# Performance work log

Measured on AMD Instinct MI355X. Metric: run time of the kernel, lower is better.

Reference implementation:

```python
import jax, jax.numpy as jnp
import numpy as np

N_NODES = 50000
N_GRAPHS = 64


def gcn_conv(x, W, b, row, col, norm, n):
    # PyG GCNConv: h = x @ W; out[i] = sum_{(j,i) in E+selfloops} norm_ji * h[j] + b
    h = x @ W
    msg = norm[:, None] * h[row]
    out = jax.ops.segment_sum(msg, col, num_segments=n)
    return out + b


def setup_inputs() -> dict:
    key = jax.random.key(0)
    ks = jax.random.split(key, 12)
    F_in, H, C = 128, 128, 16
    x = jax.random.normal(ks[0], (N_NODES, F_in), dtype=jnp.float32)
    edge_index = jax.random.randint(ks[1], (2, 800000), 0, N_NODES, dtype=jnp.int64)
    batch = jnp.sort(jax.random.randint(ks[2], (N_NODES,), 0, N_GRAPHS, dtype=jnp.int64))
    def glorot(k, shape):
        lim = np.sqrt(6.0 / (shape[0] + shape[1]))
        return jax.random.uniform(k, shape, jnp.float32, -lim, lim)
    return {
        "x": x,
        "edge_index": edge_index,
        "batch": batch,
        "W0": glorot(ks[3], (F_in, H)), "b0": jnp.zeros((H,), jnp.float32),
        "W1": glorot(ks[4], (H, H)),   "b1": jnp.zeros((H,), jnp.float32),
        "W2": glorot(ks[5], (H, H)),   "b2": jnp.zeros((H,), jnp.float32),
        "lin_W": glorot(ks[6], (H, C)),
        "lin_b": jnp.zeros((C,), jnp.float32),
    }


def reference(x, edge_index, batch, W0, b0, W1, b1, W2, b2, lin_W, lin_b):
    n = x.shape[0]
    # add self-loops
    loops = jnp.arange(n, dtype=edge_index.dtype)
    row = jnp.concatenate([edge_index[0], loops])
    col = jnp.concatenate([edge_index[1], loops])
    # symmetric normalization: deg over destination (col) incl. self-loops
    deg = jax.ops.segment_sum(jnp.ones_like(col, dtype=x.dtype), col, num_segments=n)
    dinv = jnp.where(deg > 0, jax.lax.rsqrt(deg), 0.0)
    norm = dinv[row] * dinv[col]

    h = gcn_conv(x, W0, b0, row, col, norm, n)
    h = jax.nn.relu(h)
    h = gcn_conv(h, W1, b1, row, col, norm, n)
    h = jax.nn.relu(h)
    h = gcn_conv(h, W2, b2, row, col, norm, n)

    # global mean pool over graphs
    sums = jax.ops.segment_sum(h, batch, num_segments=N_GRAPHS)
    cnts = jax.ops.segment_sum(jnp.ones((n,), h.dtype), batch, num_segments=N_GRAPHS)
    pooled = sums / jnp.maximum(cnts, 1.0)[:, None]

    # dropout is identity in eval mode
    logits = pooled @ lin_W + lin_b
    return jax.nn.softmax(logits, axis=1)
```

## Files before the change

### kernel.cpp

```cpp
#include <hip/hip_runtime.h>


#define NF 128
#define MAXBUCK 512
#define CAP 2560
#define L1_CHUNK 4096
#define L1_THREADS 512
#define L1_PER_THREAD 8
#define PPG 8

typedef __attribute__((ext_vector_type(8))) short short8;
typedef __attribute__((ext_vector_type(4))) float floatx4;
typedef __attribute__((ext_vector_type(2))) float floatx2;

__device__ __forceinline__ unsigned int bf16_rne(float x) {
    unsigned int u = __float_as_uint(x);
    return (u + 0x7fffu + ((u >> 16) & 1u)) >> 16;
}
__device__ __forceinline__ unsigned int pack_bf16_rne(float x, float y) {
    return bf16_rne(x) | (bf16_rne(y) << 16);
}
__device__ __forceinline__ float bf16u_to_f32(unsigned int u) {
    return __uint_as_float(u << 16);
}

__global__ __launch_bounds__(256) void k_repack_w3(const float* __restrict__ W0,
                                                   const float* __restrict__ W1,
                                                   const float* __restrict__ W2,
                                                   unsigned short* __restrict__ whi,
                                                   unsigned short* __restrict__ wlo,
                                                   int* __restrict__ bucket_cursor) {
    if (blockIdx.x == 0) {
        for (int i = threadIdx.x; i <= MAXBUCK; i += 256) bucket_cursor[i] = 0;
    }
    int wsel = blockIdx.x >> 3;
    const float* W = (wsel == 0) ? W0 : (wsel == 1) ? W1 : W2;
    int idx = (blockIdx.x & 7) * 256 + threadIdx.x;
    int slab = wsel * NF * NF;
    int l = idx & 63;
    int t = (idx >> 6) & 7;
    int s = idx >> 9;
    int kbase = s * 32 + (l >> 4) * 8;
    int nn = t * 16 + (l & 15);
    #pragma unroll
    for (int j = 0; j < 8; ++j) {
        float w = W[(kbase + j) * NF + nn];
        unsigned int h = bf16_rne(w);
        float hf = __uint_as_float(h << 16);
        unsigned int lo = bf16_rne(w - hf);
        whi[slab + idx * 8 + j] = (unsigned short)h;
        wlo[slab + idx * 8 + j] = (unsigned short)lo;
    }
}

__global__ __launch_bounds__(L1_THREADS) void k_bucket_scatter(
        const int* __restrict__ row, const int* __restrict__ colv,
        int* __restrict__ bucket_cursor, unsigned int* __restrict__ buck_arr,
        int ne, int etot, int nbuck) {
    __shared__ unsigned int hist[MAXBUCK];
    __shared__ unsigned int lbase[MAXBUCK];
    __shared__ unsigned int lcur[MAXBUCK];
    __shared__ unsigned int runb[MAXBUCK];
    __shared__ unsigned int sa[MAXBUCK], sb[MAXBUCK];
    __shared__ unsigned int reorder[L1_CHUNK];
    int t = threadIdx.x;
    int e0 = blockIdx.x * L1_CHUNK;
    int cnt_here = min(etot - e0, L1_CHUNK);

    hist[t] = 0;
    __syncthreads();

    unsigned int myv[L1_PER_THREAD];
    #pragma unroll
    for (int j = 0; j < L1_PER_THREAD; ++j) {
        int e = e0 + j * L1_THREADS + t;
        if (e < etot) {
            int s, d;
            if (e < ne) { s = row[e]; d = colv[e]; } else { s = d = e - ne; }
            myv[j] = (unsigned int)s | ((unsigned int)d << 16);
            atomicAdd(&hist[d >> 7], 1u);
        } else myv[j] = 0xffffffffu;
    }
    __syncthreads();

    sa[t] = hist[t];
    __syncthreads();
    unsigned int* pin = sa;
    unsigned int* pout = sb;
    #pragma unroll
    for (int off = 1; off < MAXBUCK; off <<= 1) {
        pout[t] = pin[t] + ((t >= off) ? pin[t - off] : 0);
        __syncthreads();
        unsigned int* tmp = pin; pin = pout; pout = tmp;
    }
    unsigned int ex = pin[t] - hist[t];
    lbase[t] = ex;
    lcur[t]  = ex;
    if (t < nbuck && hist[t] > 0)
        runb[t] = (unsigned int)atomicAdd(&bucket_cursor[t], (int)hist[t]);
    __syncthreads();

    #pragma unroll
    for (int j = 0; j < L1_PER_THREAD; ++j) {
        unsigned int v = myv[j];
        if (v != 0xffffffffu) {
            unsigned int p = atomicAdd(&lcur[v >> 23], 1u);
            reorder[p] = v;
        }
    }
    __syncthreads();

    for (int i = t; i < cnt_here; i += L1_THREADS) {
        unsigned int v = reorder[i];
        unsigned int b = v >> 23;
        buck_arr[(size_t)b * CAP + runb[b] + ((unsigned int)i - lbase[b])] = v;
    }
}

__global__ __launch_bounds__(256) void k_fine(const unsigned int* __restrict__ buck_arr,
                                              const int* __restrict__ bucket_cursor,
                                              int* __restrict__ starts,
                                              int* __restrict__ ends,
                                              float* __restrict__ dinv,
                                              unsigned short* __restrict__ src16,
                                              int n) {
    int b = blockIdx.x;
    int base = b * CAP;
    int m = min(bucket_cursor[b], CAP);
    int node0 = b << 7;
    int nn = min(128, n - node0);
    __shared__ unsigned int cnt[128];
    __shared__ unsigned int lsc[256];
    __shared__ unsigned int lcur[128];
    __shared__ unsigned short srcbuf[CAP];
    int t = threadIdx.x;
    if (t < 128) cnt[t] = 0;
    __syncthreads();
    for (int i = t; i < m; i += 256)
        atomicAdd(&cnt[(buck_arr[base + i] >> 16) - node0], 1u);
    __syncthreads();
    unsigned int v0 = (t < 128) ? cnt[t] : 0;
    lsc[t] = v0;
    __syncthreads();
    #pragma unroll
    for (int off = 1; off < 128; off <<= 1) {
        unsigned int add = (t >= off) ? lsc[t - off] : 0;
        __syncthreads();
        lsc[t] += add;
        __syncthreads();
    }
    if (t < 128) {
        unsigned int ex = lsc[t] - v0;
        lcur[t] = ex;
        if (t < nn) {
            starts[node0 + t] = base + (int)ex;
            ends[node0 + t]   = base + (int)(ex + v0);
            dinv[node0 + t]   = rsqrtf((float)v0);
        }
    }
    __syncthreads();
    for (int i = t; i < m; i += 256) {
        unsigned int v = buck_arr[base + i];
        unsigned int p = atomicAdd(&lcur[(v >> 16) - node0], 1u);
        srcbuf[p] = (unsigned short)(v & 0xffffu);
    }
    __syncthreads();
    for (int i = t; i < m; i += 256)
        src16[base + i] = srcbuf[i];
}

__global__ __launch_bounds__(256) void k_gemm_mfma(const float* __restrict__ Af,
                                                   const unsigned short* __restrict__ Ab,
                                                   const unsigned short* __restrict__ Whi,
                                                   const unsigned short* __restrict__ Wlo,
                                                   const float* __restrict__ dinv,
                                                   unsigned char* __restrict__ Out,
                                                   int M) {
    __shared__ unsigned short As[128 * 136];
    int tid = threadIdx.x;
    int row0 = blockIdx.x * 128;

    if (Af) {
        for (int c = tid; c < 2048; c += 256) {
            int r = c >> 4, off = c & 15;
            int gr = min(row0 + r, M - 1);
            const float4* p = (const float4*)(Af + (size_t)gr * NF) + off * 2;
            float4 v0 = p[0], v1 = p[1];
            uint4 pk;
            pk.x = pack_bf16_rne(v0.x, v0.y);
            pk.y = pack_bf16_rne(v0.z, v0.w);
            pk.z = pack_bf16_rne(v1.x, v1.y);
            pk.w = pack_bf16_rne(v1.z, v1.w);
            *(uint4*)(&As[r * 136 + off * 8]) = pk;
        }
    } else {
        for (int c = tid; c < 2048; c += 256) {
            int r = c >> 4, off = c & 15;
            int gr = min(row0 + r, M - 1);
            *(uint4*)(&As[r * 136 + off * 8]) = ((const uint4*)(Ab + (size_t)gr * NF))[off];
        }
    }
    __syncthreads();

    int wave = tid >> 6, l = tid & 63;
    int q = l >> 4, c16 = l & 15;
    int wrow0 = wave * 16;

    floatx4 acc[2][8];
    #pragma unroll
    for (int h = 0; h < 2; ++h)
        #pragma unroll
        for (int t = 0; t < 8; ++t) acc[h][t] = (floatx4){0.f, 0.f, 0.f, 0.f};

    #pragma unroll
    for (int s = 0; s < 4; ++s) {
        short8 a0 = *(const short8*)(&As[(wrow0 + c16) * 136 + s * 32 + q * 8]);
        short8 a1 = *(const short8*)(&As[(64 + wrow0 + c16) * 136 + s * 32 + q * 8]);
        #pragma unroll
        for (int t = 0; t < 8; ++t) {
            short8 bh = *(const short8*)(Whi + ((size_t)((s * 8 + t) * 64 + l) * 8));
            short8 bl = *(const short8*)(Wlo + ((size_t)((s * 8 + t) * 64 + l) * 8));
            acc[0][t] = __builtin_amdgcn_mfma_f32_16x16x32_bf16(a0, bh, acc[0][t], 0, 0, 0);
            acc[0][t] = __builtin_amdgcn_mfma_f32_16x16x32_bf16(a0, bl, acc[0][t], 0, 0, 0);
            acc[1][t] = __builtin_amdgcn_mfma_f32_16x16x32_bf16(a1, bh, acc[1][t], 0, 0, 0);
            acc[1][t] = __builtin_amdgcn_mfma_f32_16x16x32_bf16(a1, bl, acc[1][t], 0, 0, 0);
        }
    }

    #pragma unroll
    for (int h = 0; h < 2; ++h) {
        float ds[4];
        #pragma unroll
        for (int i = 0; i < 4; ++i) {
            int gr = row0 + h * 64 + wrow0 + q * 4 + i;
            ds[i] = (gr < M) ? dinv[gr] : 0.f;
        }
        #pragma unroll
        for (int t = 0; t < 8; ++t) {
            #pragma unroll
            for (int i = 0; i < 4; ++i) {
                int gr = row0 + h * 64 + wrow0 + q * 4 + i;
                if (gr < M) {
                    float v = acc[h][t][i] * ds[i];
                    unsigned int pk = __builtin_amdgcn_cvt_pk_fp8_f32(v, v, 0, false);
                    Out[(size_t)gr * NF + t * 16 + c16] = (unsigned char)(pk & 0xffu);
                }
            }
        }
    }
}

__global__ __launch_bounds__(256) void k_agg_fp8(const unsigned char* __restrict__ hs8,
                                                 const int* __restrict__ starts,
                                                 const int* __restrict__ ends,
                                                 const unsigned short* __restrict__ src16,
                                                 const float* __restrict__ dinv,
                                                 const float* __restrict__ bias,
                                                 unsigned short* __restrict__ out,
                                                 int n, int do_relu) {
    int wave = threadIdx.x >> 6;
    int lane = threadIdx.x & 63;
    int node = blockIdx.x * 4 + wave;
    if (node >= n) return;
    int g = lane >> 4;
    int f = lane & 15;
    int start = starts[node], end = ends[node];

    const uint2* h2 = (const uint2*)hs8;
    float acc[8];
    #pragma unroll
    for (int j = 0; j < 8; ++j) acc[j] = 0.f;

    for (int base = start; base < end; base += 32) {
        int   sidx[8];
        float msk[8];
        #pragma unroll
        for (int j = 0; j < 8; ++j) {
            int e = base + g + 4 * j;
            bool v = e < end;
            sidx[j] = (int)src16[v ? e : start];
            msk[j]  = v ? 1.f : 0.f;
        }
        uint2 rr[8];
        #pragma unroll
        for (int j = 0; j < 8; ++j)
            rr[j] = h2[(size_t)sidx[j] * 16 + f];
        #pragma unroll
        for (int j = 0; j < 8; ++j) {
            float m = msk[j];
            floatx2 p0 = __builtin_amdgcn_cvt_pk_f32_fp8(rr[j].x, false);
            floatx2 p1 = __builtin_amdgcn_cvt_pk_f32_fp8(rr[j].x, true);
            floatx2 p2 = __builtin_amdgcn_cvt_pk_f32_fp8(rr[j].y, false);
            floatx2 p3 = __builtin_amdgcn_cvt_pk_f32_fp8(rr[j].y, true);
            acc[0] = fmaf(m, p0.x, acc[0]);
            acc[1] = fmaf(m, p0.y, acc[1]);
            acc[2] = fmaf(m, p1.x, acc[2]);
            acc[3] = fmaf(m, p1.y, acc[3]);
            acc[4] = fmaf(m, p2.x, acc[4]);
            acc[5] = fmaf(m, p2.y, acc[5]);
            acc[6] = fmaf(m, p3.x, acc[6]);
            acc[7] = fmaf(m, p3.y, acc[7]);
        }
    }

    #pragma unroll
    for (int j = 0; j < 8; ++j) {
        acc[j] += __shfl_xor(acc[j], 16);
        acc[j] += __shfl_xor(acc[j], 32);
    }

    if (g == 0) {
        float dd = dinv[node];
        float4 b0 = ((const float4*)bias)[2 * f];
        float4 b1 = ((const float4*)bias)[2 * f + 1];
        float r[8];
        r[0] = fmaf(dd, acc[0], b0.x); r[1] = fmaf(dd, acc[1], b0.y);
        r[2] = fmaf(dd, acc[2], b0.z); r[3] = fmaf(dd, acc[3], b0.w);
        r[4] = fmaf(dd, acc[4], b1.x); r[5] = fmaf(dd, acc[5], b1.y);
        r[6] = fmaf(dd, acc[6], b1.z); r[7] = fmaf(dd, acc[7], b1.w);
        if (do_relu) {
            #pragma unroll
            for (int j = 0; j < 8; ++j) r[j] = fmaxf(r[j], 0.f);
        }
        uint4 pk;
        pk.x = pack_bf16_rne(r[0], r[1]);
        pk.y = pack_bf16_rne(r[2], r[3]);
        pk.z = pack_bf16_rne(r[4], r[5]);
        pk.w = pack_bf16_rne(r[6], r[7]);
        ((uint4*)out)[(size_t)node * 16 + f] = pk;
    }
}

__global__ __launch_bounds__(128) void k_pool_partial(const unsigned short* __restrict__ h,
                                                      const int* __restrict__ batch,
                                                      float* __restrict__ pooled_part,
                                                      int n) {
    __shared__ float red[8][NF];
    int b = blockIdx.x;
    int g = b / PPG;
    int j = b % PPG;
    int t = threadIdx.x;

    int lo = 0, hi = n;
    while (lo < hi) { int mid = (lo + hi) >> 1; if (batch[mid] < g) lo = mid + 1; else hi = mid; }
    int s = lo;
    lo = s; hi = n;
    while (lo < hi) { int mid = (lo + hi) >> 1; if (batch[mid] < g + 1) lo = mid + 1; else hi = mid; }
    int e = lo;

    int len = e - s;
    int chunk = (len + PPG - 1) / PPG;
    int i0 = s + j * chunk;
    int i1 = min(e, i0 + chunk);

    int r = t >> 4, f8 = t & 15;
    float acc[8];
    #pragma unroll
    for (int k = 0; k < 8; ++k) acc[k] = 0.f;
    for (int i = i0 + r; i < i1; i += 8) {
        uint4 v = *(const uint4*)(&h[(size_t)i * NF + f8 * 8]);
        acc[0] += bf16u_to_f32(v.x & 0xffffu); acc[1] += bf16u_to_f32(v.x >> 16);
        acc[2] += bf16u_to_f32(v.y & 0xffffu); acc[3] += bf16u_to_f32(v.y >> 16);
        acc[4] += bf16u_to_f32(v.z & 0xffffu); acc[5] += bf16u_to_f32(v.z >> 16);
        acc[6] += bf16u_to_f32(v.w & 0xffffu); acc[7] += bf16u_to_f32(v.w >> 16);
    }
    #pragma unroll
    for (int k = 0; k < 8; ++k) red[r][f8 * 8 + k] = acc[k];
    __syncthreads();
    float ssum = 0.f;
    #pragma unroll
    for (int rr = 0; rr < 8; ++rr) ssum += red[rr][t];
    pooled_part[(size_t)b * NF + t] = ssum;
}

__global__ __launch_bounds__(1024) void k_head(const float* __restrict__ pooled_part,
                                               const int* __restrict__ batch,
                                               const float* __restrict__ linW,
                                               const float* __restrict__ linb,
                                               float* __restrict__ out,
                                               int n, int n_graphs) {
    __shared__ float ph[64 * NF];
    int t = threadIdx.x;
    for (int i = t; i < n_graphs * NF; i += 1024) {
        int g = i >> 7, f = i & 127;
        float s = 0.f;
        #pragma unroll
        for (int j = 0; j < PPG; ++j)
            s += pooled_part[(size_t)(g * PPG + j) * NF + f];
        ph[i] = s;
    }
    __syncthreads();

    int g = t >> 4;
    int c = t & 15;

    int lo = 0, hi = n;
    while (lo < hi) { int mid = (lo + hi) >> 1; if (batch[mid] < g) lo = mid + 1; else hi = mid; }
    int start = lo;
    lo = start; hi = n;
    while (lo < hi) { int mid = (lo + hi) >> 1; if (batch[mid] < g + 1) lo = mid + 1; else hi = mid; }
    float inv_cnt = 1.f / fmaxf((float)(lo - start), 1.f);

    float acc = linb[c];
    for (int k = 0; k < NF; ++k)
        acc += ph[g * NF + k] * inv_cnt * linW[k * 16 + c];

    float m = acc;
    #pragma unroll
    for (int s2 = 8; s2 >= 1; s2 >>= 1) m = fmaxf(m, __shfl_xor(m, s2, 16));
    float e = expf(acc - m);
    float ssum = e;
    #pragma unroll
    for (int s2 = 8; s2 >= 1; s2 >>= 1) ssum += __shfl_xor(ssum, s2, 16);
    out[g * 16 + c] = e / ssum;
}

extern "C" void kernel_launch(void* const* d_in, const int* in_sizes, int n_in,
                              void* d_out, int out_size, void* d_ws, size_t ws_size,
                              hipStream_t stream) {
    const float* x    = (const float*)d_in[0];
    const int*   edge = (const int*)d_in[1];
    const int*   batch= (const int*)d_in[2];
    const float* W0   = (const float*)d_in[3];
    const float* b0   = (const float*)d_in[4];
    const float* W1   = (const float*)d_in[5];
    const float* b1   = (const float*)d_in[6];
    const float* W2   = (const float*)d_in[7];
    const float* b2   = (const float*)d_in[8];
    const float* linW = (const float*)d_in[9];
    const float* linb = (const float*)d_in[10];

    int n  = in_sizes[0] / NF;
    int ne = in_sizes[1] / 2;
    int n_graphs = out_size / 16;
    const int* row  = edge;
    const int* colv = edge + ne;
    int etot = ne + n;
    int nbuck = (n + 127) >> 7;

    char* p = (char*)d_ws;
    auto alloc = [&](size_t bytes) { char* r = p; p += (bytes + 255) & ~(size_t)255; return r; };
    int*   bucket_cursor = (int*)alloc((size_t)(MAXBUCK + 1) * 4);
    unsigned int* buck_arr = (unsigned int*)alloc((size_t)MAXBUCK * CAP * 4);
    unsigned short* src16  = (unsigned short*)alloc((size_t)MAXBUCK * CAP * 2);
    int*   starts  = (int*)  alloc((size_t)n * 4);
    int*   ends    = (int*)  alloc((size_t)n * 4);
    float* dinv    = (float*)alloc((size_t)n * 4);
    unsigned char*  gbuf8 = (unsigned char*) alloc((size_t)n * NF);
    unsigned short* abuf  = (unsigned short*)alloc((size_t)n * NF * 2);
    float* pooled_part = (float*)alloc((size_t)n_graphs * PPG * NF * 4);
    unsigned short* whi = (unsigned short*)alloc((size_t)3 * NF * NF * 2);
    unsigned short* wlo = (unsigned short*)alloc((size_t)3 * NF * NF * 2);

    k_repack_w3<<<24, 256, 0, stream>>>(W0, W1, W2, whi, wlo, bucket_cursor);

    k_bucket_scatter<<<(etot + L1_CHUNK - 1) / L1_CHUNK, L1_THREADS, 0, stream>>>(
        row, colv, bucket_cursor, buck_arr, ne, etot, nbuck);
    k_fine<<<nbuck, 256, 0, stream>>>(buck_arr, bucket_cursor, starts, ends, dinv, src16, n);

    int gemm_blocks = (n + 127) / 128;
    int agg_blocks  = (n + 3) / 4;
    const size_t WSLAB = (size_t)NF * NF;

    k_gemm_mfma<<<gemm_blocks, 256, 0, stream>>>(x, nullptr, whi, wlo, dinv, gbuf8, n);
    k_agg_fp8  <<<agg_blocks, 256, 0, stream>>>(gbuf8, starts, ends, src16, dinv, b0, abuf, n, 1);
    k_gemm_mfma<<<gemm_blocks, 256, 0, stream>>>(nullptr, abuf, whi + WSLAB, wlo + WSLAB, dinv, gbuf8, n);
    k_agg_fp8  <<<agg_blocks, 256, 0, stream>>>(gbuf8, starts, ends, src16, dinv, b1, abuf, n, 1);
    k_gemm_mfma<<<gemm_blocks, 256, 0, stream>>>(nullptr, abuf, whi + 2 * WSLAB, wlo + 2 * WSLAB, dinv, gbuf8, n);
    k_agg_fp8  <<<agg_blocks, 256, 0, stream>>>(gbuf8, starts, ends, src16, dinv, b2, abuf, n, 0);

    k_pool_partial<<<n_graphs * PPG, 128, 0, stream>>>(abuf, batch, pooled_part, n);
    k_head<<<1, 1024, 0, stream>>>(pooled_part, batch, linW, linb, (float*)d_out, n, n_graphs);
}
```

Baseline: 277.2 us.

## Fuse CSR finalize with first GEMM and merge pooling with head

```diff
diff --git a/kernel.cpp b/kernel.cpp
--- a/kernel.cpp
+++ b/kernel.cpp
@@ -7,7 +7,6 @@
 #define L1_CHUNK 4096
 #define L1_THREADS 512
 #define L1_PER_THREAD 8
-#define PPG 8
 
 typedef __attribute__((ext_vector_type(8))) short short8;
 typedef __attribute__((ext_vector_type(4))) float floatx4;
@@ -117,68 +116,15 @@
     }
 }
 
-__global__ __launch_bounds__(256) void k_fine(const unsigned int* __restrict__ buck_arr,
-                                              const int* __restrict__ bucket_cursor,
-                                              int* __restrict__ starts,
-                                              int* __restrict__ ends,
-                                              float* __restrict__ dinv,
-                                              unsigned short* __restrict__ src16,
-                                              int n) {
-    int b = blockIdx.x;
-    int base = b * CAP;
-    int m = min(bucket_cursor[b], CAP);
-    int node0 = b << 7;
-    int nn = min(128, n - node0);
-    __shared__ unsigned int cnt[128];
-    __shared__ unsigned int lsc[256];
-    __shared__ unsigned int lcur[128];
-    __shared__ unsigned short srcbuf[CAP];
-    int t = threadIdx.x;
-    if (t < 128) cnt[t] = 0;
-    __syncthreads();
-    for (int i = t; i < m; i += 256)
-        atomicAdd(&cnt[(buck_arr[base + i] >> 16) - node0], 1u);
-    __syncthreads();
-    unsigned int v0 = (t < 128) ? cnt[t] : 0;
-    lsc[t] = v0;
-    __syncthreads();
-    #pragma unroll
-    for (int off = 1; off < 128; off <<= 1) {
-        unsigned int add = (t >= off) ? lsc[t - off] : 0;
-        __syncthreads();
-        lsc[t] += add;
-        __syncthreads();
-    }
-    if (t < 128) {
-        unsigned int ex = lsc[t] - v0;
-        lcur[t] = ex;
-        if (t < nn) {
-            starts[node0 + t] = base + (int)ex;
-            ends[node0 + t]   = base + (int)(ex + v0);
-            dinv[node0 + t]   = rsqrtf((float)v0);
-        }
-    }
-    __syncthreads();
-    for (int i = t; i < m; i += 256) {
-        unsigned int v = buck_arr[base + i];
-        unsigned int p = atomicAdd(&lcur[(v >> 16) - node0], 1u);
-        srcbuf[p] = (unsigned short)(v & 0xffffu);
-    }
-    __syncthreads();
-    for (int i = t; i < m; i += 256)
-        src16[base + i] = srcbuf[i];
-}
-
-__global__ __launch_bounds__(256) void k_gemm_mfma(const float* __restrict__ Af,
-                                                   const unsigned short* __restrict__ Ab,
-                                                   const unsigned short* __restrict__ Whi,
-                                                   const unsigned short* __restrict__ Wlo,
-                                                   const float* __restrict__ dinv,
-                                                   unsigned char* __restrict__ Out,
-                                                   int M) {
-    __shared__ unsigned short As[128 * 136];
+__device__ __forceinline__ void gemm_tile(unsigned short* As,
+                                          const float* __restrict__ Af,
+                                          const unsigned short* __restrict__ Ab,
+                                          const unsigned short* __restrict__ Whi,
+                                          const unsigned short* __restrict__ Wlo,
+                                          unsigned char* __restrict__ Out,
+                                          int M, int tile) {
     int tid = threadIdx.x;
-    int row0 = blockIdx.x * 128;
+    int row0 = tile * 128;
 
     if (Af) {
         for (int c = tid; c < 2048; c += 256) {
@@ -229,25 +175,93 @@
 
     #pragma unroll
     for (int h = 0; h < 2; ++h) {
-        float ds[4];
-        #pragma unroll
-        for (int i = 0; i < 4; ++i) {
-            int gr = row0 + h * 64 + wrow0 + q * 4 + i;
-            ds[i] = (gr < M) ? dinv[gr] : 0.f;
-        }
         #pragma unroll
         for (int t = 0; t < 8; ++t) {
             #pragma unroll
             for (int i = 0; i < 4; ++i) {
                 int gr = row0 + h * 64 + wrow0 + q * 4 + i;
                 if (gr < M) {
-                    float v = acc[h][t][i] * ds[i];
+                    float v = acc[h][t][i];
                     unsigned int pk = __builtin_amdgcn_cvt_pk_fp8_f32(v, v, 0, false);
                     Out[(size_t)gr * NF + t * 16 + c16] = (unsigned char)(pk & 0xffu);
                 }
             }
         }
     }
+}
+
+union FgSmem {
+    struct {
+        unsigned int cnt[128]; unsigned int lsc[256]; unsigned int lcur[128];
+        unsigned short srcbuf[CAP];
+    } fi;
+    unsigned short As[128 * 136];
+};
+
+__global__ __launch_bounds__(256) void k_fine_gemm0(
+        const unsigned int* __restrict__ buck_arr,
+        const int* __restrict__ bucket_cursor,
+        int* __restrict__ starts, int* __restrict__ ends,
+        float* __restrict__ dinv, unsigned short* __restrict__ src16,
+        const float* __restrict__ x,
+        const unsigned short* __restrict__ Whi, const unsigned short* __restrict__ Wlo,
+        unsigned char* __restrict__ gbuf8,
+        int n, int nbuck) {
+    __shared__ FgSmem sm;
+    int t = threadIdx.x;
+
+    if ((int)blockIdx.x >= nbuck) {
+        gemm_tile(sm.As, x, nullptr, Whi, Wlo, gbuf8, n, blockIdx.x - nbuck);
+        return;
+    }
+
+    int b = blockIdx.x;
+    int base = b * CAP;
+    int m = min(bucket_cursor[b], CAP);
+    int node0 = b << 7;
+    int nn = min(128, n - node0);
+    if (t < 128) sm.fi.cnt[t] = 0;
+    __syncthreads();
+    for (int i = t; i < m; i += 256)
+        atomicAdd(&sm.fi.cnt[(buck_arr[base + i] >> 16) - node0], 1u);
+    __syncthreads();
+    unsigned int v0 = (t < 128) ? sm.fi.cnt[t] : 0;
+    sm.fi.lsc[t] = v0;
+    __syncthreads();
+    #pragma unroll
+    for (int off = 1; off < 128; off <<= 1) {
+        unsigned int add = (t >= off) ? sm.fi.lsc[t - off] : 0;
+        __syncthreads();
+        sm.fi.lsc[t] += add;
+        __syncthreads();
+    }
+    if (t < 128) {
+        unsigned int ex = sm.fi.lsc[t] - v0;
+        sm.fi.lcur[t] = ex;
+        if (t < nn) {
+            starts[node0 + t] = base + (int)ex;
+            ends[node0 + t]   = base + (int)(ex + v0);
+            dinv[node0 + t]   = rsqrtf((float)v0);
+        }
+    }
+    __syncthreads();
+    for (int i = t; i < m; i += 256) {
+        unsigned int v = buck_arr[base + i];
+        unsigned int p = atomicAdd(&sm.fi.lcur[(v >> 16) - node0], 1u);
+        sm.fi.srcbuf[p] = (unsigned short)(v & 0xffffu);
+    }
+    __syncthreads();
+    for (int i = t; i < m; i += 256)
+        src16[base + i] = sm.fi.srcbuf[i];
+}
+
+__global__ __launch_bounds__(256) void k_gemm_mfma(const unsigned short* __restrict__ Ab,
+                                                   const unsigned short* __restrict__ Whi,
+                                                   const unsigned short* __restrict__ Wlo,
+                                                   unsigned char* __restrict__ Out,
+                                                   int M) {
+    __shared__ unsigned short As[128 * 136];
+    gemm_tile(As, nullptr, Ab, Whi, Wlo, Out, M, blockIdx.x);
 }
 
 __global__ __launch_bounds__(256) void k_agg_fp8(const unsigned char* __restrict__ hs8,
@@ -278,8 +292,9 @@
         for (int j = 0; j < 8; ++j) {
             int e = base + g + 4 * j;
             bool v = e < end;
-            sidx[j] = (int)src16[v ? e : start];
-            msk[j]  = v ? 1.f : 0.f;
+            int si = (int)src16[v ? e : start];
+            sidx[j] = si;
+            msk[j]  = v ? dinv[si] : 0.f;
         }
         uint2 rr[8];
         #pragma unroll
@@ -331,14 +346,15 @@
     }
 }
 
-__global__ __launch_bounds__(128) void k_pool_partial(const unsigned short* __restrict__ h,
-                                                      const int* __restrict__ batch,
-                                                      float* __restrict__ pooled_part,
-                                                      int n) {
-    __shared__ float red[8][NF];
-    int b = blockIdx.x;
-    int g = b / PPG;
-    int j = b % PPG;
+__global__ __launch_bounds__(256) void k_head_pool(const unsigned short* __restrict__ h,
+                                                   const int* __restrict__ batch,
+                                                   const float* __restrict__ linW,
+                                                   const float* __restrict__ linb,
+                                                   float* __restrict__ out,
+                                                   int n) {
+    __shared__ float red[16][NF];
+    __shared__ float ph[NF];
+    int g = blockIdx.x;
     int t = threadIdx.x;
 
     int lo = 0, hi = n;
@@ -348,16 +364,11 @@
     while (lo < hi) { int mid = (lo + hi) >> 1; if (batch[mid] < g + 1) lo = mid + 1; else hi = mid; }
     int e = lo;
 
-    int len = e - s;
-    int chunk = (len + PPG - 1) / PPG;
-    int i0 = s + j * chunk;
-    int i1 = min(e, i0 + chunk);
-
     int r = t >> 4, f8 = t & 15;
     float acc[8];
     #pragma unroll
     for (int k = 0; k < 8; ++k) acc[k] = 0.f;
-    for (int i = i0 + r; i < i1; i += 8) {
+    for (int i = s + r; i < e; i += 16) {
         uint4 v = *(const uint4*)(&h[(size_t)i * NF + f8 * 8]);
         acc[0] += bf16u_to_f32(v.x & 0xffffu); acc[1] += bf16u_to_f32(v.x >> 16);
         acc[2] += bf16u_to_f32(v.y & 0xffffu); acc[3] += bf16u_to_f32(v.y >> 16);
@@ -367,52 +378,28 @@
     #pragma unroll
     for (int k = 0; k < 8; ++k) red[r][f8 * 8 + k] = acc[k];
     __syncthreads();
-    float ssum = 0.f;
-    #pragma unroll
-    for (int rr = 0; rr < 8; ++rr) ssum += red[rr][t];
-    pooled_part[(size_t)b * NF + t] = ssum;
-}
-
-__global__ __launch_bounds__(1024) void k_head(const float* __restrict__ pooled_part,
-                                               const int* __restrict__ batch,
-                                               const float* __restrict__ linW,
-                                               const float* __restrict__ linb,
-                                               float* __restrict__ out,
-                                               int n, int n_graphs) {
-    __shared__ float ph[64 * NF];
-    int t = threadIdx.x;
-    for (int i = t; i < n_graphs * NF; i += 1024) {
-        int g = i >> 7, f = i & 127;
-        float s = 0.f;
-        #pragma unroll
-        for (int j = 0; j < PPG; ++j)
-            s += pooled_part[(size_t)(g * PPG + j) * NF + f];
-        ph[i] = s;
-    }
-    __syncthreads();
-
-    int g = t >> 4;
-    int c = t & 15;
-
-    int lo = 0, hi = n;
-    while (lo < hi) { int mid = (lo + hi) >> 1; if (batch[mid] < g) lo = mid + 1; else hi = mid; }
-    int start = lo;
-    lo = start; hi = n;
-    while (lo < hi) { int mid = (lo + hi) >> 1; if (batch[mid] < g + 1) lo = mid + 1; else hi = mid; }
-    float inv_cnt = 1.f / fmaxf((float)(lo - start), 1.f);
-
-    float acc = linb[c];
-    for (int k = 0; k < NF; ++k)
-        acc += ph[g * NF + k] * inv_cnt * linW[k * 16 + c];
-
-    float m = acc;
-    #pragma unroll
-    for (int s2 = 8; s2 >= 1; s2 >>= 1) m = fmaxf(m, __shfl_xor(m, s2, 16));
-    float e = expf(acc - m);
-    float ssum = e;
-    #pragma unroll
-    for (int s2 = 8; s2 >= 1; s2 >>= 1) ssum += __shfl_xor(ssum, s2, 16);
-    out[g * 16 + c] = e / ssum;
+    if (t < NF) {
+        float ssum = 0.f;
+        #pragma unroll
+        for (int rr = 0; rr < 16; ++rr) ssum += red[rr][t];
+        ph[t] = ssum;
+    }
+    __syncthreads();
+
+    if (t < 16) {
+        float inv_cnt = 1.f / fmaxf((float)(e - s), 1.f);
+        float acc2 = linb[t];
+        for (int k = 0; k < NF; ++k)
+            acc2 += ph[k] * inv_cnt * linW[k * 16 + t];
+        float m = acc2;
+        #pragma unroll
+        for (int s2 = 8; s2 >= 1; s2 >>= 1) m = fmaxf(m, __shfl_xor(m, s2, 16));
+        float ee = expf(acc2 - m);
+        float ssum = ee;
+        #pragma unroll
+        for (int s2 = 8; s2 >= 1; s2 >>= 1) ssum += __shfl_xor(ssum, s2, 16);
+        out[g * 16 + t] = ee / ssum;
+    }
 }
 
 extern "C" void kernel_launch(void* const* d_in, const int* in_sizes, int n_in,
@@ -448,7 +435,6 @@
     float* dinv    = (float*)alloc((size_t)n * 4);
     unsigned char*  gbuf8 = (unsigned char*) alloc((size_t)n * NF);
     unsigned short* abuf  = (unsigned short*)alloc((size_t)n * NF * 2);
-    float* pooled_part = (float*)alloc((size_t)n_graphs * PPG * NF * 4);
     unsigned short* whi = (unsigned short*)alloc((size_t)3 * NF * NF * 2);
     unsigned short* wlo = (unsigned short*)alloc((size_t)3 * NF * NF * 2);
 
@@ -456,19 +442,20 @@
 
     k_bucket_scatter<<<(etot + L1_CHUNK - 1) / L1_CHUNK, L1_THREADS, 0, stream>>>(
         row, colv, bucket_cursor, buck_arr, ne, etot, nbuck);
-    k_fine<<<nbuck, 256, 0, stream>>>(buck_arr, bucket_cursor, starts, ends, dinv, src16, n);
 
     int gemm_blocks = (n + 127) / 128;
     int agg_blocks  = (n + 3) / 4;
     const size_t WSLAB = (size_t)NF * NF;
 
-    k_gemm_mfma<<<gemm_blocks, 256, 0, stream>>>(x, nullptr, whi, wlo, dinv, gbuf8, n);
+    k_fine_gemm0<<<nbuck + gemm_blocks, 256, 0, stream>>>(
+        buck_arr, bucket_cursor, starts, ends, dinv, src16,
+        x, whi, wlo, gbuf8, n, nbuck);
+
     k_agg_fp8  <<<agg_blocks, 256, 0, stream>>>(gbuf8, starts, ends, src16, dinv, b0, abuf, n, 1);
-    k_gemm_mfma<<<gemm_blocks, 256, 0, stream>>>(nullptr, abuf, whi + WSLAB, wlo + WSLAB, dinv, gbuf8, n);
+    k_gemm_mfma<<<gemm_blocks, 256, 0, stream>>>(abuf, whi + WSLAB, wlo + WSLAB, gbuf8, n);
     k_agg_fp8  <<<agg_blocks, 256, 0, stream>>>(gbuf8, starts, ends, src16, dinv, b1, abuf, n, 1);
-    k_gemm_mfma<<<gemm_blocks, 256, 0, stream>>>(nullptr, abuf, whi + 2 * WSLAB, wlo + 2 * WSLAB, dinv, gbuf8, n);
+    k_gemm_mfma<<<gemm_blocks, 256, 0, stream>>>(abuf, whi + 2 * WSLAB, wlo + 2 * WSLAB, gbuf8, n);
     k_agg_fp8  <<<agg_blocks, 256, 0, stream>>>(gbuf8, starts, ends, src16, dinv, b2, abuf, n, 0);
 
-    k_pool_partial<<<n_graphs * PPG, 128, 0, stream>>>(abuf, batch, pooled_part, n);
-    k_head<<<1, 1024, 0, stream>>>(pooled_part, batch, linW, linb, (float*)d_out, n, n_graphs);
-}
+    k_head_pool<<<n_graphs, 256, 0, stream>>>(abuf, batch, linW, linb, (float*)d_out, n);
+}
```

Measured after the change: 277.0 us. Within noise of the previous version (-0.1%).
